# Performance work log

Hardware: AMD Instinct MI355X
Metric: run time of the kernel (lower is better)

## Reference

```python
import jax, jax.numpy as jnp
import numpy as np

N_NODES = 50000

def _gcn_norm(edge_index, num_nodes):
    # PyG gcn_norm with add_self_loops=True, edge_weight=1
    src = jnp.concatenate([edge_index[0], jnp.arange(num_nodes, dtype=edge_index.dtype)])
    dst = jnp.concatenate([edge_index[1], jnp.arange(num_nodes, dtype=edge_index.dtype)])
    deg = jax.ops.segment_sum(jnp.ones(src.shape[0], dtype=jnp.float32), dst, num_segments=num_nodes)
    dis = jnp.where(deg > 0, jax.lax.rsqrt(jnp.maximum(deg, 1e-12)), 0.0)
    norm = dis[src] * dis[dst]  # [E+N]
    return src, dst, norm

def _gcn_layer(x, src, dst, norm, W, b, num_nodes):
    # x' = x @ W^T; out_i = sum_{(j->i)} norm_e * x'_j + b
    xw = x @ W.T                      # [N, h]
    msg = xw[src] * norm[:, None]     # [E+N, h] gathered + scaled messages
    out = jax.ops.segment_sum(msg, dst, num_segments=num_nodes)
    return out + b

def setup_inputs() -> dict:
    key = jax.random.key(0)
    k1, k2, k3, k4 = jax.random.split(key, 4)
    h = 128
    E = 600000
    embeddings = jax.random.normal(k1, (N_NODES, h), dtype=jnp.float32)
    edge_index = jax.random.randint(k2, (2, E), 0, N_NODES, dtype=jnp.int64)
    scale = 1.0 / np.sqrt(h)
    W1 = jax.random.normal(k3, (h, h), dtype=jnp.float32) * scale
    W2 = jax.random.normal(k4, (h, h), dtype=jnp.float32) * scale
    b1 = jnp.zeros((h,), dtype=jnp.float32)
    b2 = jnp.zeros((h,), dtype=jnp.float32)
    return {"embeddings": embeddings, "edge_index": edge_index,
            "W1": W1, "b1": b1, "W2": W2, "b2": b2}

def reference(embeddings, edge_index, W1, b1, W2, b2):
    src, dst, norm = _gcn_norm(edge_index, N_NODES)
    x = _gcn_layer(embeddings, src, dst, norm, W1, b1, N_NODES)
    x = _gcn_layer(x, src, dst, norm, W2, b2, N_NODES)
    return x
```

## Files before the change

kernel.cpp:

```cpp
#include <hip/hip_runtime.h>

typedef unsigned short u16;
typedef unsigned int   u32;

#define H    128
#define PAD  64
#define LROW 136
#define MT   32

typedef __attribute__((ext_vector_type(8))) short bf16x8;
typedef __attribute__((ext_vector_type(4))) float f32x4;

__device__ __forceinline__ float bfbits2f(u32 bits16) {
  union { float f; u32 u; } c; c.u = bits16 << 16; return c.f;
}
__device__ __forceinline__ u16 f2bf(float f) {
  union { float f; u32 u; } c; c.f = f;
  u32 u = c.u;
  return (u16)((u + 0x7fffu + ((u >> 16) & 1u)) >> 16);
}
__device__ __forceinline__ u32 fbits(float f) {
  union { float f; u32 u; } c; c.f = f; return c.u;
}

__device__ __forceinline__ void acc8(float* a, uint4 v) {
  a[0] += bfbits2f(v.x & 0xffffu); a[1] += bfbits2f(v.x >> 16);
  a[2] += bfbits2f(v.y & 0xffffu); a[3] += bfbits2f(v.y >> 16);
  a[4] += bfbits2f(v.z & 0xffffu); a[5] += bfbits2f(v.z >> 16);
  a[6] += bfbits2f(v.w & 0xffffu); a[7] += bfbits2f(v.w >> 16);
}

__global__ void k_init(int* __restrict__ cnt, int N,
                       const float* __restrict__ W1, u16* __restrict__ W1h, u16* __restrict__ W1l,
                       const float* __restrict__ W2, u16* __restrict__ W2h, u16* __restrict__ W2l) {
  int i = blockIdx.x * blockDim.x + threadIdx.x;
  if (i < N) cnt[i] = 0;
  if (i < H * H) {
    float w1 = W1[i];
    u16 h1 = f2bf(w1);
    W1h[i] = h1; W1l[i] = f2bf(w1 - bfbits2f(h1));
    float w2 = W2[i];
    u16 h2 = f2bf(w2);
    W2h[i] = h2; W2l[i] = f2bf(w2 - bfbits2f(h2));
  }
}

__global__ void k_scatter(const int* __restrict__ srcA, const int* __restrict__ dstA,
                          int* __restrict__ cnt, u16* __restrict__ slot, int E, int N) {
  int e = blockIdx.x * blockDim.x + threadIdx.x;
  if (e < E) {
    int s = srcA[e], d = dstA[e];
    s = s < 0 ? 0 : (s >= N ? N - 1 : s);
    d = d < 0 ? 0 : (d >= N ? N - 1 : d);
    int pos = atomicAdd(&cnt[d], 1);
    if (pos < PAD) slot[(size_t)d * PAD + pos] = (u16)s;
  }
}

__global__ __launch_bounds__(256) void k_prep_x(
    const float2* __restrict__ x, const int* __restrict__ cnt,
    float* __restrict__ dis, u32* __restrict__ xs, u32* __restrict__ xs2,
    u16* __restrict__ slot, int n) {
  int lane = threadIdx.x & 63;
  int node = blockIdx.x * 4 + (threadIdx.x >> 6);
  if (node > n) return;
  if (node == n) {
    xs [(size_t)n * 64 + lane] = 0u;
    xs2[(size_t)n * 64 + lane] = 0u;
    return;
  }
  int cv = cnt[node];
  float d = rsqrtf((float)(cv + 1));
  if (lane == 0) dis[node] = d;
  float2 v = x[(size_t)node * 64 + lane];
  xs[(size_t)node * 64 + lane] = (u32)f2bf(d * v.x) | ((u32)f2bf(d * v.y) << 16);
  int cc = cv > PAD ? PAD : cv;
  if (lane >= cc) slot[(size_t)node * PAD + lane] = (u16)n;
}

template <bool BF16OUT>
__global__ __launch_bounds__(512, 8) void k_layer(
    const u32* __restrict__ xs, const int* __restrict__ cntp,
    const u16* __restrict__ slot, const float* __restrict__ dis,
    const u16* __restrict__ Wh, const u16* __restrict__ Wl,
    const float* __restrict__ bias, void* __restrict__ outv, int n) {
  __shared__ u16 lyh[MT * LROW];
  __shared__ u16 lyl[MT * LROW];
  int wv = threadIdx.x >> 6;
  int lane = threadIdx.x & 63;
  int mBase = blockIdx.x * MT;
  int r = lane & 15, q = lane >> 4;

  int n0 = mBase + wv * 4;
  int qb = lane & 48;
  int c  = r;
  int nq = n0 + q; nq = nq < n ? nq : n - 1;
  int sreg[4];
#pragma unroll
  for (int b = 0; b < 4; ++b)
    sreg[b] = (int)slot[(size_t)nq * PAD + b * 16 + c];
  int cq = cntp[nq]; cq = cq > PAD ? PAD : cq;
  int m1 = __shfl(cq, lane ^ 16, 64); int t1 = cq > m1 ? cq : m1;
  int m2 = __shfl(t1, lane ^ 32, 64); int tmax = t1 > m2 ? t1 : m2;

  float A[8] = {0.f,0.f,0.f,0.f,0.f,0.f,0.f,0.f};
  uint4 sv = *(const uint4*)(xs + (size_t)nq * 64 + c * 4);
  acc8(A, sv);
#pragma unroll
  for (int b = 0; b < 4; ++b) {
    if (b * 16 >= tmax) break;
    int jend = tmax - b * 16; jend = jend > 16 ? 16 : jend;
    int sr = sreg[b];
    for (int j = 0; j < jend; j += 4) {
      int s0 = __shfl(sr, qb + j + 0, 64);
      int s1 = __shfl(sr, qb + j + 1, 64);
      int s2 = __shfl(sr, qb + j + 2, 64);
      int s3 = __shfl(sr, qb + j + 3, 64);
      uint4 v0 = *(const uint4*)(xs + (size_t)s0 * 64 + c * 4);
      uint4 v1 = *(const uint4*)(xs + (size_t)s1 * 64 + c * 4);
      uint4 v2 = *(const uint4*)(xs + (size_t)s2 * 64 + c * 4);
      uint4 v3 = *(const uint4*)(xs + (size_t)s3 * 64 + c * 4);
      acc8(A, v0);
      acc8(A, v1);
      acc8(A, v2);
      acc8(A, v3);
    }
  }
  {
    float dd = dis[nq];
    u32 u[8];
#pragma unroll
    for (int k = 0; k < 8; ++k) { A[k] *= dd; u[k] = fbits(A[k]); }
    uint4 oh, ol;
    oh.x = (u[0] >> 16) | (u[1] & 0xffff0000u);
    oh.y = (u[2] >> 16) | (u[3] & 0xffff0000u);
    oh.z = (u[4] >> 16) | (u[5] & 0xffff0000u);
    oh.w = (u[6] >> 16) | (u[7] & 0xffff0000u);
    u32 l[8];
#pragma unroll
    for (int k = 0; k < 8; ++k) l[k] = fbits(A[k] - bfbits2f(u[k] >> 16));
    ol.x = (l[0] >> 16) | (l[1] & 0xffff0000u);
    ol.y = (l[2] >> 16) | (l[3] & 0xffff0000u);
    ol.z = (l[4] >> 16) | (l[5] & 0xffff0000u);
    ol.w = (l[6] >> 16) | (l[7] & 0xffff0000u);
    int lrow = wv * 4 + q;
    *(uint4*)&lyh[lrow * LROW + c * 8] = oh;
    *(uint4*)&lyl[lrow * LROW + c * 8] = ol;
  }
  __syncthreads();

  bf16x8 Bh[4], Bl[4];
#pragma unroll
  for (int ks = 0; ks < 4; ++ks) {
    size_t boff = (size_t)(wv * 16 + r) * H + ks * 32 + q * 8;
    Bh[ks] = *(const bf16x8*)(Wh + boff);
    Bl[ks] = *(const bf16x8*)(Wl + boff);
  }
  float bv = bias[wv * 16 + r];
  int col0 = wv * 16 + r;
#pragma unroll
  for (int rt = 0; rt < 2; ++rt) {
    f32x4 acc = (f32x4){0.f, 0.f, 0.f, 0.f};
#pragma unroll
    for (int ks = 0; ks < 4; ++ks) {
      int off = (rt * 16 + r) * LROW + ks * 32 + q * 8;
      bf16x8 Ah = *(const bf16x8*)&lyh[off];
      bf16x8 Al = *(const bf16x8*)&lyl[off];
      acc = __builtin_amdgcn_mfma_f32_16x16x32_bf16(Ah, Bh[ks], acc, 0, 0, 0);
      acc = __builtin_amdgcn_mfma_f32_16x16x32_bf16(Al, Bh[ks], acc, 0, 0, 0);
      acc = __builtin_amdgcn_mfma_f32_16x16x32_bf16(Ah, Bl[ks], acc, 0, 0, 0);
    }
#pragma unroll
    for (int g = 0; g < 4; ++g) {
      int row = mBase + rt * 16 + q * 4 + g;
      if (row < n) {
        float v = acc[g] + bv;
        if (BF16OUT) {
          float dd = dis[row];
          ((u16*)outv)[(size_t)row * H + col0] = f2bf(dd * v);
        } else {
          ((float*)outv)[(size_t)row * H + col0] = v;
        }
      }
    }
  }
}

extern "C" void kernel_launch(void* const* d_in, const int* in_sizes, int n_in,
                              void* d_out, int out_size, void* d_ws, size_t ws_size,
                              hipStream_t stream) {
  const float* x0 = (const float*)d_in[0];
  const int*   ei = (const int*)d_in[1];
  const float* W1 = (const float*)d_in[2];
  const float* b1 = (const float*)d_in[3];
  const float* W2 = (const float*)d_in[4];
  const float* b2 = (const float*)d_in[5];
  int N = in_sizes[0] / H;
  int E = in_sizes[1] / 2;
  const int* srcA = ei;
  const int* dstA = ei + E;

  char* w = (char*)d_ws;
  auto alloc = [&](size_t bytes) -> void* {
    void* p = (void*)w; w += (bytes + 255) & ~(size_t)255; return p;
  };
  int*   cnt  = (int*)  alloc((size_t)N * 4);
  float* dis  = (float*)alloc((size_t)N * 4);
  u16*   slot = (u16*)  alloc((size_t)N * PAD * 2);
  u32*   xs   = (u32*)  alloc((size_t)(N + 1) * 64 * 4);
  u32*   xs2  = (u32*)  alloc((size_t)(N + 1) * 64 * 4);
  u16*   W1h  = (u16*)  alloc((size_t)H * H * 2);
  u16*   W1l  = (u16*)  alloc((size_t)H * H * 2);
  u16*   W2h  = (u16*)  alloc((size_t)H * H * 2);
  u16*   W2l  = (u16*)  alloc((size_t)H * H * 2);

  k_init   <<<(N + 255) / 256, 256, 0, stream>>>(cnt, N, W1, W1h, W1l, W2, W2h, W2l);
  k_scatter<<<(E + 255) / 256, 256, 0, stream>>>(srcA, dstA, cnt, slot, E, N);
  k_prep_x <<<(N + 4) / 4, 256, 0, stream>>>((const float2*)x0, cnt, dis, xs, xs2, slot, N);

  k_layer<true><<<(N + MT - 1) / MT, 512, 0, stream>>>(
      xs, cnt, slot, dis, W1h, W1l, b1, (void*)xs2, N);
  k_layer<false><<<(N + MT - 1) / MT, 512, 0, stream>>>(
      xs2, cnt, slot, dis, W2h, W2l, b2, d_out, N);
}
```

Before: 194.7 us.

## Split bf16 feature table into four column slabs for cache-friendly gathers

Stores the bf16 node features as four column-sliced slabs of 32 features each, so every gathered row is 64 bytes instead of 256. The aggregation loop now walks the slabs one after another, loading one u32 per lane and unrolling eight neighbours per step. The aim is a smaller working set per pass, so each slab of roughly 3.2MB stays resident in cache across gathers. In exchange, neighbour indices are reshuffled and reloaded four times, and the per-lane loads become narrow 4-byte accesses instead of 16-byte vectors.

```diff
diff --git a/kernel.cpp b/kernel.cpp
--- a/kernel.cpp
+++ b/kernel.cpp
@@ -21,13 +21,6 @@
 }
 __device__ __forceinline__ u32 fbits(float f) {
   union { float f; u32 u; } c; c.f = f; return c.u;
-}
-
-__device__ __forceinline__ void acc8(float* a, uint4 v) {
-  a[0] += bfbits2f(v.x & 0xffffu); a[1] += bfbits2f(v.x >> 16);
-  a[2] += bfbits2f(v.y & 0xffffu); a[3] += bfbits2f(v.y >> 16);
-  a[4] += bfbits2f(v.z & 0xffffu); a[5] += bfbits2f(v.z >> 16);
-  a[6] += bfbits2f(v.w & 0xffffu); a[7] += bfbits2f(v.w >> 16);
 }
 
 __global__ void k_init(int* __restrict__ cnt, int N,
@@ -64,16 +57,17 @@
   int lane = threadIdx.x & 63;
   int node = blockIdx.x * 4 + (threadIdx.x >> 6);
   if (node > n) return;
+  size_t idx = ((size_t)(lane >> 4) * (n + 1) + node) * 16 + (lane & 15);
   if (node == n) {
-    xs [(size_t)n * 64 + lane] = 0u;
-    xs2[(size_t)n * 64 + lane] = 0u;
+    xs [idx] = 0u;
+    xs2[idx] = 0u;
     return;
   }
   int cv = cnt[node];
   float d = rsqrtf((float)(cv + 1));
   if (lane == 0) dis[node] = d;
   float2 v = x[(size_t)node * 64 + lane];
-  xs[(size_t)node * 64 + lane] = (u32)f2bf(d * v.x) | ((u32)f2bf(d * v.y) << 16);
+  xs[idx] = (u32)f2bf(d * v.x) | ((u32)f2bf(d * v.y) << 16);
   int cc = cv > PAD ? PAD : cv;
   if (lane >= cc) slot[(size_t)node * PAD + lane] = (u16)n;
 }
@@ -102,50 +96,54 @@
   int cq = cntp[nq]; cq = cq > PAD ? PAD : cq;
   int m1 = __shfl(cq, lane ^ 16, 64); int t1 = cq > m1 ? cq : m1;
   int m2 = __shfl(t1, lane ^ 32, 64); int tmax = t1 > m2 ? t1 : m2;
-
-  float A[8] = {0.f,0.f,0.f,0.f,0.f,0.f,0.f,0.f};
-  uint4 sv = *(const uint4*)(xs + (size_t)nq * 64 + c * 4);
-  acc8(A, sv);
-#pragma unroll
-  for (int b = 0; b < 4; ++b) {
-    if (b * 16 >= tmax) break;
-    int jend = tmax - b * 16; jend = jend > 16 ? 16 : jend;
-    int sr = sreg[b];
-    for (int j = 0; j < jend; j += 4) {
-      int s0 = __shfl(sr, qb + j + 0, 64);
-      int s1 = __shfl(sr, qb + j + 1, 64);
-      int s2 = __shfl(sr, qb + j + 2, 64);
-      int s3 = __shfl(sr, qb + j + 3, 64);
-      uint4 v0 = *(const uint4*)(xs + (size_t)s0 * 64 + c * 4);
-      uint4 v1 = *(const uint4*)(xs + (size_t)s1 * 64 + c * 4);
-      uint4 v2 = *(const uint4*)(xs + (size_t)s2 * 64 + c * 4);
-      uint4 v3 = *(const uint4*)(xs + (size_t)s3 * 64 + c * 4);
-      acc8(A, v0);
-      acc8(A, v1);
-      acc8(A, v2);
-      acc8(A, v3);
+  float dd = dis[nq];
+  int lrow = wv * 4 + q;
+  size_t spitch = (size_t)(n + 1) * 16;
+
+#pragma unroll 1
+  for (int s = 0; s < 4; ++s) {
+    const u32* xp = xs + (size_t)s * spitch;
+    float a0 = 0.f, a1 = 0.f;
+    u32 sv = xp[(size_t)nq * 16 + c];
+    a0 += bfbits2f(sv & 0xffffu); a1 += bfbits2f(sv >> 16);
+#pragma unroll
+    for (int b = 0; b < 4; ++b) {
+      if (b * 16 >= tmax) break;
+      int jend = tmax - b * 16; jend = jend > 16 ? 16 : jend;
+      int sr = sreg[b];
+      for (int j = 0; j < jend; j += 8) {
+        int s0 = __shfl(sr, qb + j + 0, 64);
+        int s1 = __shfl(sr, qb + j + 1, 64);
+        int s2 = __shfl(sr, qb + j + 2, 64);
+        int s3 = __shfl(sr, qb + j + 3, 64);
+        int s4 = __shfl(sr, qb + j + 4, 64);
+        int s5 = __shfl(sr, qb + j + 5, 64);
+        int s6 = __shfl(sr, qb + j + 6, 64);
+        int s7 = __shfl(sr, qb + j + 7, 64);
+        u32 e0 = xp[(size_t)s0 * 16 + c];
+        u32 e1 = xp[(size_t)s1 * 16 + c];
+        u32 e2 = xp[(size_t)s2 * 16 + c];
+        u32 e3 = xp[(size_t)s3 * 16 + c];
+        u32 e4 = xp[(size_t)s4 * 16 + c];
+        u32 e5 = xp[(size_t)s5 * 16 + c];
+        u32 e6 = xp[(size_t)s6 * 16 + c];
+        u32 e7 = xp[(size_t)s7 * 16 + c];
+        a0 += bfbits2f(e0 & 0xffffu); a1 += bfbits2f(e0 >> 16);
+        a0 += bfbits2f(e1 & 0xffffu); a1 += bfbits2f(e1 >> 16);
+        a0 += bfbits2f(e2 & 0xffffu); a1 += bfbits2f(e2 >> 16);
+        a0 += bfbits2f(e3 & 0xffffu); a1 += bfbits2f(e3 >> 16);
+        a0 += bfbits2f(e4 & 0xffffu); a1 += bfbits2f(e4 >> 16);
+        a0 += bfbits2f(e5 & 0xffffu); a1 += bfbits2f(e5 >> 16);
+        a0 += bfbits2f(e6 & 0xffffu); a1 += bfbits2f(e6 >> 16);
+        a0 += bfbits2f(e7 & 0xffffu); a1 += bfbits2f(e7 >> 16);
+      }
     }
-  }
-  {
-    float dd = dis[nq];
-    u32 u[8];
-#pragma unroll
-    for (int k = 0; k < 8; ++k) { A[k] *= dd; u[k] = fbits(A[k]); }
-    uint4 oh, ol;
-    oh.x = (u[0] >> 16) | (u[1] & 0xffff0000u);
-    oh.y = (u[2] >> 16) | (u[3] & 0xffff0000u);
-    oh.z = (u[4] >> 16) | (u[5] & 0xffff0000u);
-    oh.w = (u[6] >> 16) | (u[7] & 0xffff0000u);
-    u32 l[8];
-#pragma unroll
-    for (int k = 0; k < 8; ++k) l[k] = fbits(A[k] - bfbits2f(u[k] >> 16));
-    ol.x = (l[0] >> 16) | (l[1] & 0xffff0000u);
-    ol.y = (l[2] >> 16) | (l[3] & 0xffff0000u);
-    ol.z = (l[4] >> 16) | (l[5] & 0xffff0000u);
-    ol.w = (l[6] >> 16) | (l[7] & 0xffff0000u);
-    int lrow = wv * 4 + q;
-    *(uint4*)&lyh[lrow * LROW + c * 8] = oh;
-    *(uint4*)&lyl[lrow * LROW + c * 8] = ol;
+    float f0 = a0 * dd, f1 = a1 * dd;
+    u32 u0 = fbits(f0), u1 = fbits(f1);
+    u32 l0 = fbits(f0 - bfbits2f(u0 >> 16));
+    u32 l1 = fbits(f1 - bfbits2f(u1 >> 16));
+    ((u32*)lyh)[lrow * (LROW / 2) + s * 16 + c] = (u0 >> 16) | (u1 & 0xffff0000u);
+    ((u32*)lyl)[lrow * (LROW / 2) + s * 16 + c] = (l0 >> 16) | (l1 & 0xffff0000u);
   }
   __syncthreads();
 
@@ -176,8 +174,9 @@
       if (row < n) {
         float v = acc[g] + bv;
         if (BF16OUT) {
-          float dd = dis[row];
-          ((u16*)outv)[(size_t)row * H + col0] = f2bf(dd * v);
+          float d2 = dis[row];
+          ((u16*)outv)[((size_t)(col0 >> 5) * (n + 1) + row) * 32 + (col0 & 31)]
+              = f2bf(d2 * v);
         } else {
           ((float*)outv)[(size_t)row * H + col0] = v;
         }
```

After: 209.9 us. 7.8% more time.
